# Optimization experiments

Measured on AMD Instinct MI355X. Metric: run time of the kernel, lower is better.

Reference implementation:

```python
import jax, jax.numpy as jnp
import numpy as np

EMB = 1024
FF = 1024
EPS = 1e-5

def _layernorm(x, g, b):
    mu = jnp.mean(x, axis=-1, keepdims=True)
    var = jnp.mean((x - mu) ** 2, axis=-1, keepdims=True)
    return (x - mu) * jax.lax.rsqrt(var + EPS) * g + b

def setup_inputs() -> dict:
    key = jax.random.key(0)
    ks = jax.random.split(key, 12)
    s = 1.0 / np.sqrt(EMB)
    x = jax.random.normal(ks[0], (4, 2048, EMB), dtype=jnp.float32)
    Wq = jax.random.normal(ks[1], (EMB, EMB), dtype=jnp.float32) * s
    bq = jnp.zeros((EMB,), jnp.float32)
    Wk = jax.random.normal(ks[2], (EMB, EMB), dtype=jnp.float32) * s
    bk = jnp.zeros((EMB,), jnp.float32)
    Wv = jax.random.normal(ks[3], (EMB, EMB), dtype=jnp.float32) * s
    bv = jnp.zeros((EMB,), jnp.float32)
    Wo = jax.random.normal(ks[4], (EMB, EMB), dtype=jnp.float32) * s
    bo = jnp.zeros((EMB,), jnp.float32)
    W1 = jax.random.normal(ks[5], (EMB, FF), dtype=jnp.float32) * s
    b1 = jnp.zeros((FF,), jnp.float32)
    W2 = jax.random.normal(ks[6], (FF, EMB), dtype=jnp.float32) * (1.0 / np.sqrt(FF))
    b2 = jnp.zeros((EMB,), jnp.float32)
    g1 = jnp.ones((EMB,), jnp.float32); be1 = jnp.zeros((EMB,), jnp.float32)
    g2 = jnp.ones((EMB,), jnp.float32); be2 = jnp.zeros((EMB,), jnp.float32)
    return {"x": x, "Wq": Wq, "bq": bq, "Wk": Wk, "bk": bk, "Wv": Wv, "bv": bv,
            "Wo": Wo, "bo": bo, "W1": W1, "b1": b1, "W2": W2, "b2": b2,
            "g1": g1, "be1": be1, "g2": g2, "be2": be2}

def reference(x, Wq, bq, Wk, bk, Wv, bv, Wo, bo, W1, b1, W2, b2, g1, be1, g2, be2):
    # pre-norm single-head self-attention + residual + FFN (dropout = identity, eval)
    xn = _layernorm(x, g1, be1)
    q = xn @ Wq + bq
    k = xn @ Wk + bk
    v = xn @ Wv + bv
    scores = jnp.einsum('bse,bte->bst', q, k) / jnp.sqrt(jnp.float32(EMB))
    w = jax.nn.softmax(scores, axis=-1)              # [B,S,S]
    attn = jnp.einsum('bst,bte->bse', w, v) @ Wo + bo
    x2 = x + attn
    xn2 = _layernorm(x2, g2, be2)
    ff = jax.nn.relu(xn2 @ W1 + b1) @ W2 + b2
    out = x2 + ff
    return (out, w)
```

## Files before the change

kernel.cpp:

```cpp
#include <hip/hip_runtime.h>

typedef __attribute__((ext_vector_type(8))) __bf16 bf16x8;
typedef __attribute__((ext_vector_type(4))) float f32x4;
typedef __attribute__((ext_vector_type(8))) ushort ushort8;

#define GLP(p) ((const __attribute__((address_space(1))) void*)(p))
#define LDP(p) ((__attribute__((address_space(3))) void*)(p))

__device__ __forceinline__ ushort f2b(float f) {
  union { float f; uint u; } c; c.f = f;
  uint u = c.u;
  uint r = (u + 0x7fffu + ((u >> 16) & 1u)) >> 16;
  return (ushort)r;
}

__device__ __forceinline__ void xcd_tiles(int& tileN, int& tileM) {
  const int gx = gridDim.x;
  const int nwg = gx * gridDim.y;
  int id = blockIdx.x + gx * blockIdx.y;
  id = (id & 7) * (nwg >> 3) + (id >> 3);
  tileN = (id % gx) * 128;
  tileM = (id / gx) * 128;
}

__device__ __forceinline__ float block_reduce_sum(float v, float* sm) {
#pragma unroll
  for (int off = 1; off < 64; off <<= 1) v += __shfl_xor(v, off);
  const int wave = threadIdx.x >> 6, lane = threadIdx.x & 63;
  __syncthreads();
  if (lane == 0) sm[wave] = v;
  __syncthreads();
  return sm[0] + sm[1] + sm[2] + sm[3];
}

__global__ __launch_bounds__(256) void wtrans6_kernel(
    const float* __restrict__ W0, const float* __restrict__ W1,
    const float* __restrict__ W2, const float* __restrict__ W3,
    const float* __restrict__ W4, const float* __restrict__ W5,
    ushort* __restrict__ T0, ushort* __restrict__ T1, ushort* __restrict__ T2,
    ushort* __restrict__ T3, ushort* __restrict__ T4, ushort* __restrict__ T5) {
  __shared__ float tile[32][33];
  const float* Ws[6] = {W0, W1, W2, W3, W4, W5};
  ushort* Ts[6] = {T0, T1, T2, T3, T4, T5};
  const float* W = Ws[blockIdx.z];
  ushort* Wt = Ts[blockIdx.z];
  const int K = 1024, N = 1024;
  const int n0 = blockIdx.x * 32, k0 = blockIdx.y * 32;
  const int tx = threadIdx.x, ty = threadIdx.y;
#pragma unroll
  for (int i = 0; i < 32; i += 8)
    tile[ty + i][tx] = W[(long)(k0 + ty + i) * N + n0 + tx];
  __syncthreads();
#pragma unroll
  for (int i = 0; i < 32; i += 8)
    Wt[(long)(n0 + ty + i) * K + k0 + tx] = f2b(tile[tx][ty + i]);
}

__global__ __launch_bounds__(256) void layernorm_kernel(
    const float* __restrict__ x, const float* __restrict__ g,
    const float* __restrict__ be, ushort* __restrict__ out) {
  __shared__ float sm[4];
  const long row = blockIdx.x;
  const float4 v = reinterpret_cast<const float4*>(x + row * 1024)[threadIdx.x];
  float s = v.x + v.y + v.z + v.w;
  s = block_reduce_sum(s, sm);
  const float mu = s * (1.0f / 1024.0f);
  const float dx = v.x - mu, dy = v.y - mu, dz = v.z - mu, dw = v.w - mu;
  float s2 = dx * dx + dy * dy + dz * dz + dw * dw;
  s2 = block_reduce_sum(s2, sm);
  const float rstd = rsqrtf(s2 * (1.0f / 1024.0f) + 1e-5f);
  const float4 gg = reinterpret_cast<const float4*>(g)[threadIdx.x];
  const float4 bb = reinterpret_cast<const float4*>(be)[threadIdx.x];
  ushort4 o;
  o.x = f2b(dx * rstd * gg.x + bb.x);
  o.y = f2b(dy * rstd * gg.y + bb.y);
  o.z = f2b(dz * rstd * gg.z + bb.z);
  o.w = f2b(dw * rstd * gg.w + bb.w);
  reinterpret_cast<ushort4*>(out + row * 1024)[threadIdx.x] = o;
}

__global__ __launch_bounds__(256) void softmax_kernel(
    float* __restrict__ s, ushort* __restrict__ wb) {
  __shared__ float sm[4];
  const long row = blockIdx.x;
  float4* r4 = reinterpret_cast<float4*>(s + row * 2048);
  float4 v0 = r4[threadIdx.x * 2];
  float4 v1 = r4[threadIdx.x * 2 + 1];
  float m = fmaxf(fmaxf(fmaxf(v0.x, v0.y), fmaxf(v0.z, v0.w)),
                  fmaxf(fmaxf(v1.x, v1.y), fmaxf(v1.z, v1.w)));
#pragma unroll
  for (int off = 1; off < 64; off <<= 1) m = fmaxf(m, __shfl_xor(m, off));
  const int wave = threadIdx.x >> 6, lane = threadIdx.x & 63;
  if (lane == 0) sm[wave] = m;
  __syncthreads();
  m = fmaxf(fmaxf(sm[0], sm[1]), fmaxf(sm[2], sm[3]));
  v0.x = expf(v0.x - m); v0.y = expf(v0.y - m);
  v0.z = expf(v0.z - m); v0.w = expf(v0.w - m);
  v1.x = expf(v1.x - m); v1.y = expf(v1.y - m);
  v1.z = expf(v1.z - m); v1.w = expf(v1.w - m);
  float sum = v0.x + v0.y + v0.z + v0.w + v1.x + v1.y + v1.z + v1.w;
  sum = block_reduce_sum(sum, sm);
  const float inv = 1.0f / sum;
  v0.x *= inv; v0.y *= inv; v0.z *= inv; v0.w *= inv;
  v1.x *= inv; v1.y *= inv; v1.z *= inv; v1.w *= inv;
  r4[threadIdx.x * 2] = v0;
  r4[threadIdx.x * 2 + 1] = v1;
  ushort8 o;
  o[0] = f2b(v0.x); o[1] = f2b(v0.y); o[2] = f2b(v0.z); o[3] = f2b(v0.w);
  o[4] = f2b(v1.x); o[5] = f2b(v1.y); o[6] = f2b(v1.z); o[7] = f2b(v1.w);
  *reinterpret_cast<ushort8*>(wb + row * 2048 + threadIdx.x * 8) = o;
}

#define EP_BF16 1
#define EP_F32 2
#define EP_BIAS 4
#define EP_RELU 8
#define EP_SCALE 16
#define EP_RESID 32
#define EP_TRANS 64

template <int FLAGS>
__global__ __launch_bounds__(512) void gemm_bt(
    const ushort* __restrict__ A, const ushort* __restrict__ Bt,
    float* __restrict__ Cf, ushort* __restrict__ Cb,
    const float* __restrict__ bias, const float* __restrict__ resid,
    int M, int N, int K, float scale, long sA, long sB, long sC) {
  A += (long)blockIdx.z * sA;
  Bt += (long)blockIdx.z * sB;
  const long coff = (long)blockIdx.z * sC;
  int tileN, tileM;
  xcd_tiles(tileN, tileM);
  const int tid = threadIdx.x, lane = tid & 63, wid = tid >> 6;
  const int wm = wid >> 2, wn = wid & 3;
  __shared__ alignas(16) ushort As[4][128][32];
  __shared__ alignas(16) ushort Bs[4][128][32];
  f32x4 acc[4][2] = {};

  const int srow = wid * 16 + (lane >> 2);
  const int scol = (lane & 3) * 8;
  const ushort* aP = A + (long)(tileM + srow) * K + scol;
  const ushort* bP = Bt + (long)(tileN + srow) * K + scol;

#define STAGE(slot, kk)                                                                  \
  do {                                                                                   \
    __builtin_amdgcn_global_load_lds(GLP(aP + (kk)), LDP(&As[slot][wid * 16][0]), 16, 0, \
                                     0);                                                 \
    __builtin_amdgcn_global_load_lds(GLP(bP + (kk)), LDP(&Bs[slot][wid * 16][0]), 16, 0, \
                                     0);                                                 \
  } while (0)

  STAGE(0, 0);
  STAGE(1, 32);
  __syncthreads();
  int cur = 0;
  for (int kk = 0; kk < K; kk += 64) {
    const int nxt = cur ^ 2;
    if (kk + 64 < K) {
      STAGE(nxt, kk + 64);
      STAGE(nxt + 1, kk + 96);
    }
#pragma unroll
    for (int u = 0; u < 2; ++u) {
      const int sl = cur + u;
      bf16x8 a[4], b[2];
#pragma unroll
      for (int m = 0; m < 4; ++m)
        a[m] = *reinterpret_cast<const bf16x8*>(
            &As[sl][wm * 64 + m * 16 + (lane & 15)][(lane >> 4) * 8]);
#pragma unroll
      for (int n = 0; n < 2; ++n)
        b[n] = *reinterpret_cast<const bf16x8*>(
            &Bs[sl][wn * 32 + n * 16 + (lane & 15)][(lane >> 4) * 8]);
#pragma unroll
      for (int m = 0; m < 4; ++m)
#pragma unroll
        for (int n = 0; n < 2; ++n)
          acc[m][n] = __builtin_amdgcn_mfma_f32_16x16x32_bf16(a[m], b[n], acc[m][n], 0, 0, 0);
    }
    __syncthreads();
    cur = nxt;
  }
#undef STAGE

  const int row0 = tileM + wm * 64 + ((lane >> 4) << 2);
  const int col0 = tileN + wn * 32 + (lane & 15);
#pragma unroll
  for (int n = 0; n < 2; ++n) {
    const int col = col0 + n * 16;
    const float bv = (FLAGS & EP_BIAS) ? bias[col] : 0.0f;
#pragma unroll
    for (int m = 0; m < 4; ++m) {
#pragma unroll
      for (int i = 0; i < 4; ++i) {
        const int row = row0 + m * 16 + i;
        float v = acc[m][n][i];
        if (FLAGS & EP_SCALE) v *= scale;
        v += bv;
        if (FLAGS & EP_RELU) v = fmaxf(v, 0.0f);
        if (FLAGS & EP_RESID) v += resid[coff + (long)row * N + col];
        if (FLAGS & EP_F32) Cf[coff + (long)row * N + col] = v;
        if (FLAGS & EP_BF16) {
          if (FLAGS & EP_TRANS)
            Cb[coff + (long)col * M + row] = f2b(v);
          else
            Cb[coff + (long)row * N + col] = f2b(v);
        }
      }
    }
  }
}

__global__ __launch_bounds__(512) void gemm_qkv(
    const ushort* __restrict__ A, const ushort* __restrict__ Bt,
    ushort* __restrict__ Cq, ushort* __restrict__ Ck, ushort* __restrict__ Cv,
    const float* __restrict__ bq, const float* __restrict__ bk,
    const float* __restrict__ bv, int M, int N, int K) {
  int tileN, tileM;
  xcd_tiles(tileN, tileM);
  const int tid = threadIdx.x, lane = tid & 63, wid = tid >> 6;
  const int wm = wid >> 2, wn = wid & 3;
  __shared__ alignas(16) ushort As[4][128][32];
  __shared__ alignas(16) ushort Bs[4][128][32];
  f32x4 acc[4][2] = {};

  const int srow = wid * 16 + (lane >> 2);
  const int scol = (lane & 3) * 8;
  const ushort* aP = A + (long)(tileM + srow) * K + scol;
  const ushort* bP = Bt + (long)(tileN + srow) * K + scol;

#define STAGE(slot, kk)                                                                  \
  do {                                                                                   \
    __builtin_amdgcn_global_load_lds(GLP(aP + (kk)), LDP(&As[slot][wid * 16][0]), 16, 0, \
                                     0);                                                 \
    __builtin_amdgcn_global_load_lds(GLP(bP + (kk)), LDP(&Bs[slot][wid * 16][0]), 16, 0, \
                                     0);                                                 \
  } while (0)

  STAGE(0, 0);
  STAGE(1, 32);
  __syncthreads();
  int cur = 0;
  for (int kk = 0; kk < K; kk += 64) {
    const int nxt = cur ^ 2;
    if (kk + 64 < K) {
      STAGE(nxt, kk + 64);
      STAGE(nxt + 1, kk + 96);
    }
#pragma unroll
    for (int u = 0; u < 2; ++u) {
      const int sl = cur + u;
      bf16x8 a[4], b[2];
#pragma unroll
      for (int m = 0; m < 4; ++m)
        a[m] = *reinterpret_cast<const bf16x8*>(
            &As[sl][wm * 64 + m * 16 + (lane & 15)][(lane >> 4) * 8]);
#pragma unroll
      for (int n = 0; n < 2; ++n)
        b[n] = *reinterpret_cast<const bf16x8*>(
            &Bs[sl][wn * 32 + n * 16 + (lane & 15)][(lane >> 4) * 8]);
#pragma unroll
      for (int m = 0; m < 4; ++m)
#pragma unroll
        for (int n = 0; n < 2; ++n)
          acc[m][n] = __builtin_amdgcn_mfma_f32_16x16x32_bf16(a[m], b[n], acc[m][n], 0, 0, 0);
    }
    __syncthreads();
    cur = nxt;
  }
#undef STAGE

  const int seg = tileN >> 10;
  const float* bias = (seg == 0) ? bq : (seg == 1) ? bk : bv;
  const int row0 = tileM + wm * 64 + ((lane >> 4) << 2);
  const int col0 = tileN + wn * 32 + (lane & 15);
#pragma unroll
  for (int n = 0; n < 2; ++n) {
    const int col = col0 + n * 16;
    const int bcol = col & 1023;
    const float bvv = bias[bcol];
#pragma unroll
    for (int m = 0; m < 4; ++m) {
#pragma unroll
      for (int i = 0; i < 4; ++i) {
        const int row = row0 + m * 16 + i;
        const float v = acc[m][n][i] + bvv;
        if (seg == 0) {
          Cq[(long)row * 1024 + bcol] = f2b(v);
        } else if (seg == 1) {
          Ck[(long)row * 1024 + bcol] = f2b(v);
        } else {
          Cv[((long)(row >> 11) * 1024 + bcol) * 2048 + (row & 2047)] = f2b(v);
        }
      }
    }
  }
}

extern "C" void kernel_launch(void* const* d_in, const int* in_sizes, int n_in,
                              void* d_out, int out_size, void* d_ws, size_t ws_size,
                              hipStream_t stream) {
  const int B = 4, S = 2048, E = 1024, FFD = 1024;
  const long MS = (long)B * S;
  const float* x   = (const float*)d_in[0];
  const float* Wq  = (const float*)d_in[1];
  const float* bq  = (const float*)d_in[2];
  const float* Wk  = (const float*)d_in[3];
  const float* bk  = (const float*)d_in[4];
  const float* Wv  = (const float*)d_in[5];
  const float* bv  = (const float*)d_in[6];
  const float* Wo  = (const float*)d_in[7];
  const float* bo  = (const float*)d_in[8];
  const float* W1  = (const float*)d_in[9];
  const float* b1  = (const float*)d_in[10];
  const float* W2  = (const float*)d_in[11];
  const float* b2  = (const float*)d_in[12];
  const float* g1  = (const float*)d_in[13];
  const float* be1 = (const float*)d_in[14];
  const float* g2  = (const float*)d_in[15];
  const float* be2 = (const float*)d_in[16];

  float* out  = (float*)d_out;
  float* wout = out + MS * E;

  ushort* xnA = (ushort*)d_ws;
  ushort* qB  = xnA + MS * E;
  ushort* kC  = qB + MS * E;
  ushort* vTD = kC + MS * E;
  ushort* wE  = vTD + MS * E;
  float*  x2F = (float*)(wE + (long)B * S * S);
  ushort* wts = (ushort*)(x2F + MS * E);
  ushort* WqT = wts;
  ushort* WkT = WqT + (long)E * E;
  ushort* WvT = WkT + (long)E * E;
  ushort* WoT = WvT + (long)E * E;
  ushort* W1T = WoT + (long)E * E;
  ushort* W2T = W1T + (long)E * FFD;

  hipLaunchKernelGGL(wtrans6_kernel, dim3(E / 32, E / 32, 6), dim3(32, 8), 0, stream,
                     Wq, Wk, Wv, Wo, W1, W2, WqT, WkT, WvT, WoT, W1T, W2T);

  hipLaunchKernelGGL(layernorm_kernel, dim3(MS), dim3(256), 0, stream, x, g1, be1, xnA);

  hipLaunchKernelGGL(gemm_qkv, dim3(3 * E / 128, MS / 128, 1), dim3(512), 0, stream,
                     xnA, WqT, qB, kC, vTD, bq, bk, bv, (int)MS, 3 * E, E);

  hipLaunchKernelGGL((gemm_bt<EP_F32 | EP_SCALE>), dim3(S / 128, S / 128, B), dim3(512), 0,
                     stream, qB, kC, wout, (ushort*)nullptr, (const float*)nullptr,
                     (const float*)nullptr, S, S, E, 0.03125f, (long)S * E, (long)S * E,
                     (long)S * S);

  hipLaunchKernelGGL(softmax_kernel, dim3(B * S), dim3(256), 0, stream, wout, wE);

  hipLaunchKernelGGL((gemm_bt<EP_BF16>), dim3(E / 128, S / 128, B), dim3(512), 0, stream,
                     wE, vTD, (float*)nullptr, qB, (const float*)nullptr,
                     (const float*)nullptr, S, E, S, 1.0f, (long)S * S, (long)E * S,
                     (long)S * E);

  hipLaunchKernelGGL((gemm_bt<EP_F32 | EP_BIAS | EP_RESID>), dim3(E / 128, MS / 128, 1),
                     dim3(512), 0, stream, qB, WoT, x2F, (ushort*)nullptr, bo, x,
                     (int)MS, E, E, 1.0f, 0L, 0L, 0L);

  hipLaunchKernelGGL(layernorm_kernel, dim3(MS), dim3(256), 0, stream, x2F, g2, be2, xnA);

  hipLaunchKernelGGL((gemm_bt<EP_BF16 | EP_BIAS | EP_RELU>), dim3(FFD / 128, MS / 128, 1),
                     dim3(512), 0, stream, xnA, W1T, (float*)nullptr, kC, b1,
                     (const float*)nullptr, (int)MS, FFD, E, 1.0f, 0L, 0L, 0L);

  hipLaunchKernelGGL((gemm_bt<EP_F32 | EP_BIAS | EP_RESID>), dim3(E / 128, MS / 128, 1),
                     dim3(512), 0, stream, kC, W2T, out, (ushort*)nullptr, b2, x2F,
                     (int)MS, E, FFD, 1.0f, 0L, 0L, 0L);
}
```

Measured before the change: 329.6 us.

## Fuse exp into score GEMM and defer softmax normalization to PV epilogue

The QK^T GEMM now applies exp in its epilogue and writes bf16 exponentials directly, replacing the fp32 score write and the separate max/exp/sum softmax pass. A lighter rownorm kernel reads the bf16 exponentials, computes row sums, writes the fp32 attention weights and stores per-row inverse sums. The PV GEMM consumes the unnormalized exponentials and rescales each row in its epilogue. This cuts several full passes over the large score matrix, but drops max subtraction, so it can overflow for large scores. The returned weights also now derive from bf16 exponentials rather than fp32. The XCD tile swizzle also becomes optional per GEMM and is removed from the QKV GEMM.

Result: faster. 315.5 us (median of 2 runs) (-4.3%).

```diff
diff --git a/kernel.cpp b/kernel.cpp
--- a/kernel.cpp
+++ b/kernel.cpp
@@ -12,6 +12,10 @@
   uint u = c.u;
   uint r = (u + 0x7fffu + ((u >> 16) & 1u)) >> 16;
   return (ushort)r;
+}
+__device__ __forceinline__ float b2f(ushort b) {
+  union { uint u; float f; } c; c.u = ((uint)b) << 16;
+  return c.f;
 }
 
 __device__ __forceinline__ void xcd_tiles(int& tileN, int& tileM) {
@@ -79,36 +83,26 @@
   reinterpret_cast<ushort4*>(out + row * 1024)[threadIdx.x] = o;
 }
 
-__global__ __launch_bounds__(256) void softmax_kernel(
-    float* __restrict__ s, ushort* __restrict__ wb) {
+__global__ __launch_bounds__(256) void rownorm_kernel(
+    const ushort* __restrict__ e, float* __restrict__ w, float* __restrict__ invZ) {
   __shared__ float sm[4];
   const long row = blockIdx.x;
-  float4* r4 = reinterpret_cast<float4*>(s + row * 2048);
-  float4 v0 = r4[threadIdx.x * 2];
-  float4 v1 = r4[threadIdx.x * 2 + 1];
-  float m = fmaxf(fmaxf(fmaxf(v0.x, v0.y), fmaxf(v0.z, v0.w)),
-                  fmaxf(fmaxf(v1.x, v1.y), fmaxf(v1.z, v1.w)));
-#pragma unroll
-  for (int off = 1; off < 64; off <<= 1) m = fmaxf(m, __shfl_xor(m, off));
-  const int wave = threadIdx.x >> 6, lane = threadIdx.x & 63;
-  if (lane == 0) sm[wave] = m;
-  __syncthreads();
-  m = fmaxf(fmaxf(sm[0], sm[1]), fmaxf(sm[2], sm[3]));
-  v0.x = expf(v0.x - m); v0.y = expf(v0.y - m);
-  v0.z = expf(v0.z - m); v0.w = expf(v0.w - m);
-  v1.x = expf(v1.x - m); v1.y = expf(v1.y - m);
-  v1.z = expf(v1.z - m); v1.w = expf(v1.w - m);
-  float sum = v0.x + v0.y + v0.z + v0.w + v1.x + v1.y + v1.z + v1.w;
-  sum = block_reduce_sum(sum, sm);
-  const float inv = 1.0f / sum;
-  v0.x *= inv; v0.y *= inv; v0.z *= inv; v0.w *= inv;
-  v1.x *= inv; v1.y *= inv; v1.z *= inv; v1.w *= inv;
-  r4[threadIdx.x * 2] = v0;
-  r4[threadIdx.x * 2 + 1] = v1;
-  ushort8 o;
-  o[0] = f2b(v0.x); o[1] = f2b(v0.y); o[2] = f2b(v0.z); o[3] = f2b(v0.w);
-  o[4] = f2b(v1.x); o[5] = f2b(v1.y); o[6] = f2b(v1.z); o[7] = f2b(v1.w);
-  *reinterpret_cast<ushort8*>(wb + row * 2048 + threadIdx.x * 8) = o;
+  const ushort8 v = *reinterpret_cast<const ushort8*>(e + row * 2048 + threadIdx.x * 8);
+  float f[8];
+  float s = 0.0f;
+#pragma unroll
+  for (int i = 0; i < 8; ++i) {
+    f[i] = b2f(v[i]);
+    s += f[i];
+  }
+  s = block_reduce_sum(s, sm);
+  const float inv = 1.0f / s;
+  if (threadIdx.x == 0) invZ[row] = inv;
+  float4 o0 = {f[0] * inv, f[1] * inv, f[2] * inv, f[3] * inv};
+  float4 o1 = {f[4] * inv, f[5] * inv, f[6] * inv, f[7] * inv};
+  float4* wp = reinterpret_cast<float4*>(w + row * 2048);
+  wp[threadIdx.x * 2] = o0;
+  wp[threadIdx.x * 2 + 1] = o1;
 }
 
 #define EP_BF16 1
@@ -118,18 +112,28 @@
 #define EP_SCALE 16
 #define EP_RESID 32
 #define EP_TRANS 64
+#define EP_EXP 128
+#define EP_ROWSC 256
+#define EP_SWZ 512
 
 template <int FLAGS>
 __global__ __launch_bounds__(512) void gemm_bt(
     const ushort* __restrict__ A, const ushort* __restrict__ Bt,
     float* __restrict__ Cf, ushort* __restrict__ Cb,
     const float* __restrict__ bias, const float* __restrict__ resid,
+    const float* __restrict__ rowsc,
     int M, int N, int K, float scale, long sA, long sB, long sC) {
   A += (long)blockIdx.z * sA;
   Bt += (long)blockIdx.z * sB;
   const long coff = (long)blockIdx.z * sC;
+  const long rbase = (long)blockIdx.z * M;
   int tileN, tileM;
-  xcd_tiles(tileN, tileM);
+  if (FLAGS & EP_SWZ) {
+    xcd_tiles(tileN, tileM);
+  } else {
+    tileN = blockIdx.x * 128;
+    tileM = blockIdx.y * 128;
+  }
   const int tid = threadIdx.x, lane = tid & 63, wid = tid >> 6;
   const int wm = wid >> 2, wn = wid & 3;
   __shared__ alignas(16) ushort As[4][128][32];
@@ -197,6 +201,8 @@
         if (FLAGS & EP_SCALE) v *= scale;
         v += bv;
         if (FLAGS & EP_RELU) v = fmaxf(v, 0.0f);
+        if (FLAGS & EP_EXP) v = __expf(v);
+        if (FLAGS & EP_ROWSC) v *= rowsc[rbase + row];
         if (FLAGS & EP_RESID) v += resid[coff + (long)row * N + col];
         if (FLAGS & EP_F32) Cf[coff + (long)row * N + col] = v;
         if (FLAGS & EP_BF16) {
@@ -215,8 +221,7 @@
     ushort* __restrict__ Cq, ushort* __restrict__ Ck, ushort* __restrict__ Cv,
     const float* __restrict__ bq, const float* __restrict__ bk,
     const float* __restrict__ bv, int M, int N, int K) {
-  int tileN, tileM;
-  xcd_tiles(tileN, tileM);
+  const int tileN = blockIdx.x * 128, tileM = blockIdx.y * 128;
   const int tid = threadIdx.x, lane = tid & 63, wid = tid >> 6;
   const int wm = wid >> 2, wn = wid & 3;
   __shared__ alignas(16) ushort As[4][128][32];
@@ -335,6 +340,7 @@
   ushort* WoT = WvT + (long)E * E;
   ushort* W1T = WoT + (long)E * E;
   ushort* W2T = W1T + (long)E * FFD;
+  float*  invZ = (float*)(W2T + (long)FFD * E);
 
   hipLaunchKernelGGL(wtrans6_kernel, dim3(E / 32, E / 32, 6), dim3(32, 8), 0, stream,
                      Wq, Wk, Wv, Wo, W1, W2, WqT, WkT, WvT, WoT, W1T, W2T);
@@ -344,29 +350,33 @@
   hipLaunchKernelGGL(gemm_qkv, dim3(3 * E / 128, MS / 128, 1), dim3(512), 0, stream,
                      xnA, WqT, qB, kC, vTD, bq, bk, bv, (int)MS, 3 * E, E);
 
-  hipLaunchKernelGGL((gemm_bt<EP_F32 | EP_SCALE>), dim3(S / 128, S / 128, B), dim3(512), 0,
-                     stream, qB, kC, wout, (ushort*)nullptr, (const float*)nullptr,
-                     (const float*)nullptr, S, S, E, 0.03125f, (long)S * E, (long)S * E,
-                     (long)S * S);
-
-  hipLaunchKernelGGL(softmax_kernel, dim3(B * S), dim3(256), 0, stream, wout, wE);
-
-  hipLaunchKernelGGL((gemm_bt<EP_BF16>), dim3(E / 128, S / 128, B), dim3(512), 0, stream,
-                     wE, vTD, (float*)nullptr, qB, (const float*)nullptr,
-                     (const float*)nullptr, S, E, S, 1.0f, (long)S * S, (long)E * S,
-                     (long)S * E);
-
-  hipLaunchKernelGGL((gemm_bt<EP_F32 | EP_BIAS | EP_RESID>), dim3(E / 128, MS / 128, 1),
-                     dim3(512), 0, stream, qB, WoT, x2F, (ushort*)nullptr, bo, x,
+  hipLaunchKernelGGL((gemm_bt<EP_BF16 | EP_SCALE | EP_EXP | EP_SWZ>),
+                     dim3(S / 128, S / 128, B), dim3(512), 0, stream,
+                     qB, kC, (float*)nullptr, wE, (const float*)nullptr,
+                     (const float*)nullptr, (const float*)nullptr,
+                     S, S, E, 0.03125f, (long)S * E, (long)S * E, (long)S * S);
+
+  hipLaunchKernelGGL(rownorm_kernel, dim3(B * S), dim3(256), 0, stream, wE, wout, invZ);
+
+  hipLaunchKernelGGL((gemm_bt<EP_BF16 | EP_ROWSC | EP_SWZ>), dim3(E / 128, S / 128, B),
+                     dim3(512), 0, stream, wE, vTD, (float*)nullptr, qB,
+                     (const float*)nullptr, (const float*)nullptr, invZ,
+                     S, E, S, 1.0f, (long)S * S, (long)E * S, (long)S * E);
+
+  hipLaunchKernelGGL((gemm_bt<EP_F32 | EP_BIAS | EP_RESID | EP_SWZ>),
+                     dim3(E / 128, MS / 128, 1), dim3(512), 0, stream, qB, WoT, x2F,
+                     (ushort*)nullptr, bo, x, (const float*)nullptr,
                      (int)MS, E, E, 1.0f, 0L, 0L, 0L);
 
   hipLaunchKernelGGL(layernorm_kernel, dim3(MS), dim3(256), 0, stream, x2F, g2, be2, xnA);
 
-  hipLaunchKernelGGL((gemm_bt<EP_BF16 | EP_BIAS | EP_RELU>), dim3(FFD / 128, MS / 128, 1),
-                     dim3(512), 0, stream, xnA, W1T, (float*)nullptr, kC, b1,
-                     (const float*)nullptr, (int)MS, FFD, E, 1.0f, 0L, 0L, 0L);
-
-  hipLaunchKernelGGL((gemm_bt<EP_F32 | EP_BIAS | EP_RESID>), dim3(E / 128, MS / 128, 1),
-                     dim3(512), 0, stream, kC, W2T, out, (ushort*)nullptr, b2, x2F,
+  hipLaunchKernelGGL((gemm_bt<EP_BF16 | EP_BIAS | EP_RELU | EP_SWZ>),
+                     dim3(FFD / 128, MS / 128, 1), dim3(512), 0, stream, xnA, W1T,
+                     (float*)nullptr, kC, b1, (const float*)nullptr, (const float*)nullptr,
+                     (int)MS, FFD, E, 1.0f, 0L, 0L, 0L);
+
+  hipLaunchKernelGGL((gemm_bt<EP_F32 | EP_BIAS | EP_RESID | EP_SWZ>),
+                     dim3(E / 128, MS / 128, 1), dim3(512), 0, stream, kC, W2T, out,
+                     (ushort*)nullptr, b2, x2F, (const float*)nullptr,
                      (int)MS, E, FFD, 1.0f, 0L, 0L, 0L);
 }
```
